# Performance work log

Hardware: AMD Instinct MI355X
Metric: run time of the kernel (lower is better)

The kernel has to match this reference:

```python
import jax, jax.numpy as jnp
import numpy as np
from jax import lax
from jax.scipy.special import gammaln

B, T_FEATS, T_TEXT = 16, 2000, 400
ADIM, ODIM = 256, 512
BIG_NEG = -1e30
BLANK_LOGP = -1.0  # log(blank_prob) with blank_prob = e**-1


def _conv1d(x, w, b, pad):
    # x: (B, C_in, L), w: (C_out, C_in, K)
    y = lax.conv_general_dilated(x, w, (1,), [(pad, pad)],
                                 dimension_numbers=('NCH', 'OIH', 'NCH'))
    return y + b[None, :, None]


def _betabinom_prior(T, N):
    # ESPnet AlignmentModule beta-binomial attention prior (w=1):
    # alpha_t = t (1..T), beta_t = T - t + 1, k = 1..N, n = N
    t = jnp.arange(1, T + 1, dtype=jnp.float32)
    a = t[:, None]                                   # (T,1)
    bb = (T - t + 1.0)[:, None]                      # (T,1)
    k = jnp.arange(1, N + 1, dtype=jnp.float32)[None, :]  # (1,N)
    n = float(N)
    betaln = lambda x, y: gammaln(x) + gammaln(y) - gammaln(x + y)
    logC = gammaln(n + 1.0) - gammaln(k + 1.0) - gammaln(n - k + 1.0)
    return logC + betaln(k + a, n - k + bb) - betaln(a, bb)  # (T,N)


def _alignment_encoder(txt, speech, tw1, tb1, tw2, tb2, fw1, fb1, fw2, fb2, fw3, fb3):
    t = txt.transpose(0, 2, 1)                       # (B, adim, T_text)
    t = jax.nn.relu(_conv1d(t, tw1, tb1, 1))
    t = _conv1d(t, tw2, tb2, 0)
    t = t.transpose(0, 2, 1)                         # (B, T_text, adim)

    f = speech.transpose(0, 2, 1)                    # (B, odim, T_feats)
    f = jax.nn.relu(_conv1d(f, fw1, fb1, 1))
    f = jax.nn.relu(_conv1d(f, fw2, fb2, 1))
    f = _conv1d(f, fw3, fb3, 0)
    f = f.transpose(0, 2, 1)                         # (B, T_feats, adim)

    # score = -||f_t - t_s||_2 via expansion (avoids (B,T,S,D) intermediate)
    d2 = (jnp.sum(f * f, -1)[:, :, None] + jnp.sum(t * t, -1)[:, None, :]
          - 2.0 * jnp.einsum('btd,bsd->bts', f, t))
    score = -jnp.sqrt(jnp.maximum(d2, 1e-12))        # (B, T_feats, T_text)
    logp = jax.nn.log_softmax(score, axis=-1)
    return logp + _betabinom_prior(T_FEATS, T_TEXT)[None]


def _forwardsum_loss(log_p_attn):
    # CTC forward algorithm; targets are 1..N (all distinct) + interleaved blanks
    Bv, T, N = log_p_attn.shape
    lp = jnp.concatenate(
        [jnp.full((Bv, T, 1), BLANK_LOGP, log_p_attn.dtype), log_p_attn], axis=-1)
    lp = jax.nn.log_softmax(lp, axis=-1)             # (B, T, N+1)
    S = 2 * N + 1
    ext = np.zeros(S, np.int32); ext[1::2] = np.arange(1, N + 1)
    skip_ok = np.zeros(S, bool); skip_ok[3::2] = True  # non-blank, distinct labels
    ext = jnp.asarray(ext); skip_ok = jnp.asarray(skip_ok)

    emit = lp[:, :, ext]                             # (B, T, S)
    alpha = jnp.full((Bv, S), BIG_NEG)
    alpha = alpha.at[:, 0].set(emit[:, 0, 0]).at[:, 1].set(emit[:, 0, 1])

    def step(alpha, e):
        a1 = jnp.concatenate([jnp.full((Bv, 1), BIG_NEG), alpha[:, :-1]], axis=1)
        a2 = jnp.concatenate([jnp.full((Bv, 2), BIG_NEG), alpha[:, :-2]], axis=1)
        a2 = jnp.where(skip_ok[None, :], a2, BIG_NEG)
        alpha = jnp.logaddexp(jnp.logaddexp(alpha, a1), a2) + e
        return alpha, None

    alpha, _ = lax.scan(step, alpha, jnp.moveaxis(emit[:, 1:], 1, 0))
    nll = -jnp.logaddexp(alpha[:, -1], alpha[:, -2])  # (B,)
    # F.ctc_loss reduction='mean' divides each sample's nll by target length
    return jnp.mean(nll / N)


def _mas_single(lp):
    # lp: (T_feats, T_text) -> monotonic alignment (T_feats,) int32
    log_prob = lp.T                                  # (N, T)
    N, T = T_TEXT, T_FEATS
    q0 = jnp.where(jnp.arange(N) == 0, log_prob[0, 0], BIG_NEG)

    def fwd(q, col):
        q = jnp.maximum(q, jnp.concatenate([jnp.full((1,), BIG_NEG), q[:-1]])) + col
        return q, q

    _, qs = lax.scan(fwd, q0, log_prob[:, 1:].T)     # (T-1, N)
    Q = lax.stop_gradient(jnp.concatenate([q0[None], qs], axis=0))  # (T, N)

    def bwd(a_next, q_col):
        i_a = jnp.maximum(a_next - 1, 0)
        a = jnp.where(a_next == 0, 0,
                      jnp.where(q_col[i_a] >= q_col[a_next], i_a, a_next))
        a = a.astype(jnp.int32)
        return a, a

    _, A_rev = lax.scan(bwd, jnp.array(N - 1, jnp.int32), Q[:-1], reverse=True)
    return jnp.concatenate([A_rev, jnp.array([N - 1], jnp.int32)])  # (T,)


def _viterbi_decode(log_p_attn):
    A = jax.vmap(_mas_single)(log_p_attn)            # (B, T_feats) int32
    ds = jax.vmap(lambda a: jnp.bincount(a, length=T_TEXT))(A)
    ds = ds.astype(log_p_attn.dtype)                 # (B, T_text) durations
    gathered = jnp.take_along_axis(log_p_attn, A[:, :, None], axis=2)[..., 0]
    bin_loss = -jnp.mean(jnp.mean(gathered, axis=1))
    return ds, bin_loss


def setup_inputs() -> dict:
    key = jax.random.key(0)
    ks = jax.random.split(key, 12)
    s = 0.05
    inp = {
        'speech': jax.random.normal(ks[0], (B, T_FEATS, ODIM), jnp.float32),
        'txt': jax.random.normal(ks[1], (B, T_TEXT, ADIM), jnp.float32),
        'speech_len': jnp.full((B,), T_FEATS, jnp.int32),
        'txt_len': jnp.full((B,), T_TEXT, jnp.int32),
        'tw1': jax.random.normal(ks[2], (ADIM, ADIM, 3)) * s,
        'tb1': jnp.zeros((ADIM,)),
        'tw2': jax.random.normal(ks[3], (ADIM, ADIM, 1)) * s,
        'tb2': jnp.zeros((ADIM,)),
        'fw1': jax.random.normal(ks[4], (ADIM, ODIM, 3)) * s,
        'fb1': jnp.zeros((ADIM,)),
        'fw2': jax.random.normal(ks[5], (ADIM, ADIM, 3)) * s,
        'fb2': jnp.zeros((ADIM,)),
        'fw3': jax.random.normal(ks[6], (ADIM, ADIM, 1)) * s,
        'fb3': jnp.zeros((ADIM,)),
    }
    return inp


def reference(speech, txt, speech_len, txt_len,
              tw1, tb1, tw2, tb2, fw1, fb1, fw2, fb2, fw3, fb3):
    # lengths are full (no padding), so masks are no-ops
    log_p_attn = _alignment_encoder(txt, speech, tw1, tb1, tw2, tb2,
                                    fw1, fb1, fw2, fb2, fw3, fb3)
    forwardsum_loss = _forwardsum_loss(log_p_attn)
    ds, bin_loss = _viterbi_decode(log_p_attn)
    return ds, bin_loss, forwardsum_loss, log_p_attn
```

## Files before the change

### kernel.cpp

```cpp
#include <hip/hip_runtime.h>
#include <math.h>

typedef unsigned int u32;
typedef unsigned long long u64;
typedef unsigned short u16;
typedef __attribute__((ext_vector_type(8))) _Float16 f16x8;
typedef __attribute__((ext_vector_type(4))) float f32x4;

#define BIGN (-1e30f)

static constexpr int NB = 16;
static constexpr int TF = 2000;
static constexpr int TT = 400;

__device__ __forceinline__ float wsum(float v){
#pragma unroll
  for(int o=32;o;o>>=1) v += __shfl_xor(v,o,64);
  return v;
}
__device__ __forceinline__ float EXP2(float x){ return __builtin_amdgcn_exp2f(x); }
__device__ __forceinline__ float LOG2(float x){ return __builtin_amdgcn_logf(x); }
__device__ __forceinline__ float lse2b(float x, float y){
  float m = fmaxf(x,y);
  return m + LOG2(1.0f + EXP2(-fabsf(x-y)));
}
__device__ __forceinline__ float lse3b(float x, float y, float z){
  float mx = fmaxf(fmaxf(x,y),z);
  float md = __builtin_amdgcn_fmed3f(x,y,z);
  float mn = fminf(fminf(x,y),z);
  return mx + LOG2(1.0f + EXP2(md-mx) + EXP2(mn-mx));
}
__device__ __forceinline__ u16 f2h(float v){
  _Float16 h = (_Float16)v;
  return *(u16*)&h;
}
__device__ __forceinline__ float shup1(float v){
  int r = __builtin_amdgcn_update_dpp(__float_as_int(BIGN), __float_as_int(v),
                                      0x138, 0xf, 0xf, false);
  return __int_as_float(r);
}

__global__ void k_lgt(double* lgt){
  int m = blockIdx.x*blockDim.x + threadIdx.x;
  if(m < 2432) lgt[m] = (m>=1)? lgamma((double)m) : 0.0;
}
__global__ void k_terms(const double* __restrict__ lgt, double* rowA, double* colA, double* sA){
  int i = blockIdx.x*blockDim.x + threadIdx.x;
  if(i < TF)   rowA[i] = -lgt[2401] - lgt[i+1] - lgt[2000-i] + lgt[2001];
  if(i < TT)   colA[i] =  lgt[401]  - lgt[i+2] - lgt[400-i];
  if(i < 2399) sA[i]   =  lgt[i+2]  + lgt[2399-i];
}

__device__ __forceinline__ void packf(const float* __restrict__ w, u16* __restrict__ dst,
    int CIN, int KW, int i){
  int k = i % KW;
  int c = (i / KW) % CIN;
  int o = i / (KW*CIN);
  dst[((size_t)k*256 + o)*CIN + c] = f2h(w[i]);
}
__device__ __forceinline__ void cvtp(const float* __restrict__ src, u16* __restrict__ dst,
    int P, int C, int i){
  int c = i % C;
  int p = (i / C) % (P+2);
  int b = i / (C*(P+2));
  float v = 0.f;
  if(p>=1 && p<=P) v = src[((size_t)b*P + (p-1))*C + c];
  dst[i] = f2h(v);
}
__device__ __forceinline__ void zpr(u16* __restrict__ buf, int P, int j){
  int c = j % 256;
  int s = (j / 256) & 1;
  int b = j / 512;
  buf[((size_t)b*(P+2) + (s? P+1 : 0))*256 + c] = 0;
}
__global__ __launch_bounds__(256) void prep1_k(
    const float* __restrict__ fw1, const float* __restrict__ fw2, const float* __restrict__ fw3,
    const float* __restrict__ tw1, const float* __restrict__ tw2, const float* __restrict__ txt,
    u16* fw1p, u16* fw2p, u16* fw3p, u16* tw1p, u16* tw2p,
    u16* inbfT, u16* tout1, u16* out1){
  constexpr int N = 393216+196608+65536+196608+65536+1646592+8192+8192;
  for(int i = blockIdx.x*256 + threadIdx.x; i < N; i += gridDim.x*256){
    int j = i;
    if(j < 393216){ packf(fw1, fw1p, 512, 3, j); continue; } j -= 393216;
    if(j < 196608){ packf(fw2, fw2p, 256, 3, j); continue; } j -= 196608;
    if(j < 65536) { packf(fw3, fw3p, 256, 1, j); continue; } j -= 65536;
    if(j < 196608){ packf(tw1, tw1p, 256, 3, j); continue; } j -= 196608;
    if(j < 65536) { packf(tw2, tw2p, 256, 1, j); continue; } j -= 65536;
    if(j < 1646592){ cvtp(txt, inbfT, TT, 256, j); continue; } j -= 1646592;
    if(j < 8192) { zpr(tout1, TT, j); continue; } j -= 8192;
    zpr(out1, TF, j);
  }
}

__global__ __launch_bounds__(256) void cvt_pad_k(const float* __restrict__ src, u16* __restrict__ dst,
    int P, int C){
  int n = NB*(P+2)*C;
  for(int i = blockIdx.x*256 + threadIdx.x; i < n; i += gridDim.x*256) cvtp(src, dst, P, C, i);
}
__global__ __launch_bounds__(256) void zpad_k(u16* __restrict__ buf, int P){
  int n = NB*2*256;
  for(int i = blockIdx.x*256 + threadIdx.x; i < n; i += gridDim.x*256) zpr(buf, P, i);
}

template<int CIN, int KW, bool RELU, bool OBF>
__global__ __launch_bounds__(256) void mfconv_k(const u16* __restrict__ inb,
    const u16* __restrict__ wp, const float* __restrict__ bias, void* __restrict__ outp, int P){
  __shared__ __align__(16) u16 Al[4*66*8];
  __shared__ __align__(16) u16 Bl[KW*4*256*8];
  const int b = blockIdx.y;
  const int m0 = blockIdx.x * 64;
  const int tid = threadIdx.x;
  const int lane = tid & 63, wv = tid >> 6;
  const int lo16 = lane & 15, hi = lane >> 4;
  constexpr int K1 = (KW==1)? 1 : 0;
  const u16* inB = inb + (size_t)b*(P+2)*CIN;
  f32x4 acc[4][4];
#pragma unroll
  for(int i=0;i<4;i++)
#pragma unroll
    for(int j=0;j<4;j++) acc[i][j] = (f32x4){0.f,0.f,0.f,0.f};

  for(int c0=0; c0<CIN; c0+=32){
    __syncthreads();
    for(int idx = tid; idx < 264; idx += 256){
      int r = idx >> 2, q = idx & 3;
      int rowp = m0 + r;
      f16x8 v = (f16x8){0,0,0,0,0,0,0,0};
      if(rowp <= P+1) v = *(const f16x8*)&inB[(size_t)rowp*CIN + c0 + q*8];
      *(f16x8*)&Al[(q*66 + r)*8] = v;
    }
#pragma unroll
    for(int k=0;k<KW;k++){
      const u16* wr = &wp[((size_t)(k*256) + tid)*CIN + c0];
      f16x8 w0 = *(const f16x8*)&wr[0];
      f16x8 w1 = *(const f16x8*)&wr[8];
      f16x8 w2 = *(const f16x8*)&wr[16];
      f16x8 w3 = *(const f16x8*)&wr[24];
      *(f16x8*)&Bl[((k*4+0)*256 + tid)*8] = w0;
      *(f16x8*)&Bl[((k*4+1)*256 + tid)*8] = w1;
      *(f16x8*)&Bl[((k*4+2)*256 + tid)*8] = w2;
      *(f16x8*)&Bl[((k*4+3)*256 + tid)*8] = w3;
    }
    __syncthreads();
#pragma unroll
    for(int k=0;k<KW;k++){
      f16x8 af[4];
#pragma unroll
      for(int rf=0;rf<4;rf++)
        af[rf] = *(const f16x8*)&Al[(hi*66 + rf*16 + lo16 + k + K1)*8];
#pragma unroll
      for(int cf=0;cf<4;cf++){
        int o = wv*64 + cf*16 + lo16;
        f16x8 bf = *(const f16x8*)&Bl[((k*4+hi)*256 + o)*8];
#pragma unroll
        for(int rf=0;rf<4;rf++)
          acc[rf][cf] = __builtin_amdgcn_mfma_f32_16x16x32_f16(af[rf], bf, acc[rf][cf], 0, 0, 0);
      }
    }
  }
#pragma unroll
  for(int cf=0;cf<4;cf++){
    int o = wv*64 + cf*16 + lo16;
    float bs = bias[o];
#pragma unroll
    for(int rf=0;rf<4;rf++){
#pragma unroll
      for(int j=0;j<4;j++){
        int p = m0 + rf*16 + hi*4 + j;
        if(p < P){
          float v = acc[rf][cf][j] + bs;
          if(RELU) v = fmaxf(v, 0.f);
          if(OBF) ((u16*)outp)[((size_t)b*(P+2) + p + 1)*256 + o] = f2h(v);
          else    ((float*)outp)[((size_t)b*P + p)*256 + o] = v;
        }
      }
    }
  }
}

__global__ __launch_bounds__(256) void norm2b_k(const float* __restrict__ x1, const float* __restrict__ x2,
    float* __restrict__ o1, float* __restrict__ o2){
  int r = blockIdx.x*4 + (threadIdx.x>>6);
  int lane = threadIdx.x & 63;
  const float* src; float* dst; int rr;
  if(r < NB*TF){ src = x1; dst = o1; rr = r; }
  else { rr = r - NB*TF; if(rr >= NB*TT) return; src = x2; dst = o2; }
  float4 v = ((const float4*)(src + (size_t)rr*256))[lane];
  float s = v.x*v.x + v.y*v.y + v.z*v.z + v.w*v.w;
  s = wsum(s);
  if(lane==0) dst[rr] = s;
}

__global__ __launch_bounds__(256) void score_gemm(const float* __restrict__ F, const float* __restrict__ Tn,
    const float* __restrict__ fn2, const float* __restrict__ tn2, float* __restrict__ outp){
  constexpr int KC = 32;
  __shared__ __align__(16) float As[KC][68];
  __shared__ __align__(16) float Bs[KC][68];
  const int b = blockIdx.z;
  const int t0 = blockIdx.y*64, s0 = blockIdx.x*64;
  const int tid = threadIdx.x, tx = tid&15, ty = tid>>4;
  const float* Fb = F  + (size_t)b*TF*256;
  const float* Tb = Tn + (size_t)b*TT*256;
  float acc[4][4] = {};
  const int lk = tid & 31, lt0 = (tid>>5)*8;
  for(int k0=0;k0<256;k0+=KC){
    __syncthreads();
#pragma unroll
    for(int i=0;i<8;i++){
      int t = t0 + lt0 + i;
      As[lk][lt0+i] = (t<TF)? Fb[(size_t)t*256 + k0 + lk] : 0.f;
      int s = s0 + lt0 + i;
      Bs[lk][lt0+i] = (s<TT)? Tb[(size_t)s*256 + k0 + lk] : 0.f;
    }
    __syncthreads();
#pragma unroll
    for(int k=0;k<KC;k++){
      float a0[4], b0[4];
      *(float4*)a0 = *(const float4*)&As[k][ty*4];
      *(float4*)b0 = *(const float4*)&Bs[k][tx*4];
#pragma unroll
      for(int i=0;i<4;i++)
#pragma unroll
        for(int j=0;j<4;j++) acc[i][j] = fmaf(a0[i], b0[j], acc[i][j]);
    }
  }
#pragma unroll
  for(int i=0;i<4;i++){
    int t = t0 + ty*4 + i;
    if(t<TF){
      float fn = fn2[b*TF + t];
#pragma unroll
      for(int j=0;j<4;j++){
        int s = s0 + tx*4 + j;
        if(s<TT){
          float d2 = fn + tn2[b*TT + s] - 2.f*acc[i][j];
          outp[((size_t)b*TF + t)*TT + s] = -sqrtf(fmaxf(d2, 1e-12f));
        }
      }
    }
  }
}

__global__ __launch_bounds__(128) void softmax_prior_k(float* __restrict__ logp,
    const double* __restrict__ rowA, const double* __restrict__ colA, const double* __restrict__ sA,
    float* __restrict__ Z2){
  const int row = blockIdx.x;
  const int t0 = row % TF;
  float* rp = logp + (size_t)row*TT;
  const int tid = threadIdx.x;
  __shared__ float sh2[2];
  float v[4]; int ix[4];
#pragma unroll
  for(int i=0;i<4;i++){ ix[i] = tid + i*128; v[i] = (ix[i]<TT)? rp[ix[i]] : BIGN; }
  float m = fmaxf(fmaxf(v[0],v[1]),fmaxf(v[2],v[3]));
#pragma unroll
  for(int o=32;o;o>>=1) m = fmaxf(m, __shfl_xor(m,o,64));
  if((tid&63)==0) sh2[tid>>6] = m;
  __syncthreads();
  m = fmaxf(sh2[0], sh2[1]);
  float s = 0.f;
#pragma unroll
  for(int i=0;i<4;i++) if(ix[i]<TT) s += __expf(v[i]-m);
  s = wsum(s);
  __syncthreads();
  if((tid&63)==0) sh2[tid>>6] = s;
  __syncthreads();
  s = sh2[0] + sh2[1];
  const float lse = m + __logf(s);
  const double rA = rowA[t0];
  float f[4]; float m2 = BIGN;
#pragma unroll
  for(int i=0;i<4;i++){
    if(ix[i]<TT){
      float pr = (float)(colA[ix[i]] + sA[t0+ix[i]] + rA);
      f[i] = (v[i]-lse) + pr;
      rp[ix[i]] = f[i];
      m2 = fmaxf(m2, f[i]);
    } else f[i] = BIGN;
  }
#pragma unroll
  for(int o=32;o;o>>=1) m2 = fmaxf(m2, __shfl_xor(m2,o,64));
  __syncthreads();
  if((tid&63)==0) sh2[tid>>6] = m2;
  __syncthreads();
  m2 = fmaxf(fmaxf(sh2[0],sh2[1]), -1.0f);
  float s2 = (tid==0)? __expf(-1.0f - m2) : 0.f;
#pragma unroll
  for(int i=0;i<4;i++) if(ix[i]<TT) s2 += __expf(f[i]-m2);
  s2 = wsum(s2);
  __syncthreads();
  if((tid&63)==0) sh2[tid>>6] = s2;
  __syncthreads();
  if(tid==0) Z2[row] = m2 + __logf(sh2[0]+sh2[1]);
}

#define LCTC8(E, KV) { \
  float bv = bnd[dir][((KV)-1)&1]; \
  float n1 = shup1(a[7]); \
  if(half && lane==0) n1 = bv; \
  float w0 = lse2b(a[0], n1); \
  float w1 = lse2b(a[2], a[1]); \
  float w2 = lse2b(a[4], a[3]); \
  float w3 = lse2b(a[6], a[5]); \
  a[7] = lse2b(a[7], w3) + (E)[3]; \
  a[5] = lse2b(a[5], w2) + (E)[2]; \
  a[3] = lse2b(a[3], w1) + (E)[1]; \
  a[1] = lse2b(a[1], w0) + (E)[0]; \
  a[6] = w3 + EBL; a[4] = w2 + EBL; a[2] = w1 + EBL; a[0] = w0 + EBL; \
  if(half==0 && lane==52) bnd[dir][(KV)&1] = a[7]; \
  __syncthreads(); }

#define CPREF4(E, K) { int kk=(K); if(kk>999) kk=999; int row = dir? (TF-1-kk) : kk; \
  const float* rpp = lp + (size_t)row*TT; \
  (E)[0]=rpp[jc[0]]*IL2; (E)[1]=rpp[jc[1]]*IL2; (E)[2]=rpp[jc[2]]*IL2; (E)[3]=rpp[jc[3]]*IL2; }

#define MAS_STEP(E, TIDX) { \
  float n1 = shup1(q[6]); \
  u32 byte = 0; \
  if(lane>0 && n1 >= q[0]) byte |= 1u; \
  if(q[0] >= q[1]) byte |= 2u; \
  if(q[1] >= q[2]) byte |= 4u; \
  if(q[2] >= q[3]) byte |= 8u; \
  if(q[3] >= q[4]) byte |= 16u; \
  if(q[4] >= q[5]) byte |= 32u; \
  if(q[5] >= q[6]) byte |= 64u; \
  cb[(size_t)((TIDX)-1)*64 + lane] = (unsigned char)byte; \
  q[6] = fmaxf(q[6], q[5]) + (E)[6]; \
  q[5] = fmaxf(q[5], q[4]) + (E)[5]; \
  q[4] = fmaxf(q[4], q[3]) + (E)[4]; \
  q[3] = fmaxf(q[3], q[2]) + (E)[3]; \
  q[2] = fmaxf(q[2], q[1]) + (E)[2]; \
  q[1] = fmaxf(q[1], q[0]) + (E)[1]; \
  q[0] = fmaxf(q[0], n1) + (E)[0]; }

#define MPREF(E, ROW) { int rr=(ROW); rr = (rr>TF-1)? (TF-1) : rr; const float* rpp = lp + (size_t)rr*TT; \
  (E)[0]=rpp[jc[0]]; (E)[1]=rpp[jc[1]]; (E)[2]=rpp[jc[2]]; (E)[3]=rpp[jc[3]]; \
  (E)[4]=rpp[jc[4]]; (E)[5]=rpp[jc[5]]; (E)[6]=rpp[jc[6]]; }

__global__ __launch_bounds__(256) __attribute__((amdgpu_waves_per_eu(1,1)))
void scan_k(const float* __restrict__ logp,
    const float* __restrict__ Z2, unsigned char* __restrict__ cmpb, float* __restrict__ nll){
  const int lane = threadIdx.x & 63;
  const int wave = threadIdx.x >> 6;
  constexpr float IL2 = 1.4426950408889634f;
  constexpr float L2  = 0.6931471805599453f;
  if(blockIdx.x < NB){
    const int b = blockIdx.x;
    const float* lp = logp + (size_t)b*TF*TT;
    __shared__ float af[801], ag[801];
    __shared__ float bnd[2][2];
    const int dir  = wave >> 1;
    const int half = wave & 1;
    const int base = half ? 424 : 0;
    double zs = 0.0;
    if(wave==0){
      for(int t=lane; t<TF; t+=64) zs += (double)Z2[b*TF + t];
#pragma unroll
      for(int o=32;o;o>>=1) zs += __shfl_xor(zs, o, 64);
    }
    int jc[4];
#pragma unroll
    for(int i=0;i<4;i++){
      int j = base/2 + 4*lane + i;
      if(dir) j = TT-1-j;
      jc[i] = (j < 0)? 0 : ((j > TT-1)? TT-1 : j);
    }
    float a[8];
#pragma unroll
    for(int i=0;i<8;i++) a[i] = BIGN;
    if(half==0 && lane==0){
      a[0] = -1.0f*IL2;
      a[1] = (dir? lp[(size_t)(TF-1)*TT + (TT-1)] : lp[0]) * IL2;
    }
    const float EBL = -1.0f*IL2;
    if(half==0 && lane==52) bnd[dir][0] = a[7];
    float e0[4],e1[4],e2[4],e3[4],e4[4],e5[4],e6[4],e7[4];
    CPREF4(e0,1); CPREF4(e1,2); CPREF4(e2,3); CPREF4(e3,4);
    CPREF4(e4,5); CPREF4(e5,6); CPREF4(e6,7); CPREF4(e7,8);
    __syncthreads();
    int k = 1;
    for(; k + 8 <= 993; k += 8){
      LCTC8(e0, k);   CPREF4(e0, k+8);
      LCTC8(e1, k+1); CPREF4(e1, k+9);
      LCTC8(e2, k+2); CPREF4(e2, k+10);
      LCTC8(e3, k+3); CPREF4(e3, k+11);
      LCTC8(e4, k+4); CPREF4(e4, k+12);
      LCTC8(e5, k+5); CPREF4(e5, k+13);
      LCTC8(e6, k+6); CPREF4(e6, k+14);
      LCTC8(e7, k+7); CPREF4(e7, k+15);
    }
    for(; k<=999; k++){
      float P[4];
      CPREF4(P, k);
      LCTC8(P, k);
    }
    float* dst = dir? ag : af;
#pragma unroll
    for(int i=0;i<8;i++){
      int s = base + 8*lane + i;
      if(half){ if(s<=800) dst[s] = a[i]; }
      else    { if(s<=423) dst[s] = a[i]; }
    }
    __syncthreads();
    if(wave==0){
      float acc = BIGN;
      for(int s = lane; s <= 800; s += 64){
        float x0 = af[s];
        float x1 = (s>=1)? af[s-1] : BIGN;
        float x2 = ((s&1) && s>=3)? af[s-2] : BIGN;
        float A1 = lse3b(x0,x1,x2);
        acc = lse2b(acc, A1 + ag[800-s]);
      }
#pragma unroll
      for(int o=32;o;o>>=1) acc = lse2b(acc, __shfl_xor(acc,o,64));
      if(lane==0) nll[b] = -((acc*L2) - (float)zs);
    }
  } else {
    if(wave) return;
    const int b = blockIdx.x - NB;
    const float* lp = logp + (size_t)b*TF*TT;
    unsigned char* cb = cmpb + (size_t)b*TF*64;
    int jc[7];
#pragma unroll
    for(int i=0;i<7;i++){ int j = 7*lane + i; jc[i] = (j < TT)? j : (TT-1); }
    float q[7];
#pragma unroll
    for(int i=0;i<7;i++) q[i] = BIGN;
    if(lane==0) q[0] = lp[0];
    float e0[7],e1[7],e2[7],e3[7];
    MPREF(e0,1); MPREF(e1,2); MPREF(e2,3); MPREF(e3,4);
    int t0 = 1;
    for(; t0 + 4 <= TF; t0 += 4){
      MAS_STEP(e0, t0);   MPREF(e0, t0+4);
      MAS_STEP(e1, t0+1); MPREF(e1, t0+5);
      MAS_STEP(e2, t0+2); MPREF(e2, t0+6);
      MAS_STEP(e3, t0+3); MPREF(e3, t0+7);
    }
    for(; t0<TF; t0++){
      float P[7];
      MPREF(P, t0);
      MAS_STEP(P, t0);
    }
    {
      float n1 = shup1(q[6]);
      u32 byte = 0;
      if(lane>0 && n1 >= q[0]) byte |= 1u;
      if(q[0] >= q[1]) byte |= 2u;
      if(q[1] >= q[2]) byte |= 4u;
      if(q[2] >= q[3]) byte |= 8u;
      if(q[3] >= q[4]) byte |= 16u;
      if(q[4] >= q[5]) byte |= 32u;
      if(q[5] >= q[6]) byte |= 64u;
      cb[(size_t)(TF-1)*64 + lane] = (unsigned char)byte;
    }
  }
}

__global__ __launch_bounds__(256) void masback_k(const unsigned char* __restrict__ cmpb,
    const float* __restrict__ logp, float* __restrict__ ds, float* __restrict__ gsum){
  const int b = blockIdx.x;
  const unsigned char* cb = cmpb + (size_t)b*TF*64;
  __shared__ unsigned char bits[500*64];
  __shared__ short Ash[TF];
  __shared__ int cnt[TT];
  __shared__ float ps[4];
  int a = TT-1;
  for(int ch=3; ch>=0; ch--){
    const int tlo = ch*500;
    __syncthreads();
    for(int i=threadIdx.x;i<8000;i+=256) ((u32*)bits)[i] = ((const u32*)(cb + (size_t)tlo*64))[i];
    __syncthreads();
    if(threadIdx.x==0){
      int thi = tlo + 499;
      if(ch==3){ Ash[TF-1] = (short)(TT-1); thi = TF-2; }
      for(int t=thi;t>=tlo;t--){
        if(a > 0){
          unsigned char w = bits[(t-tlo)*64 + a/7];
          a -= (int)((w >> (a%7)) & 1u);
        }
        Ash[t] = (short)a;
      }
    }
  }
  __syncthreads();
  for(int i=threadIdx.x;i<TT;i+=256) cnt[i]=0;
  __syncthreads();
  float part = 0.f;
  const float* lp = logp + (size_t)b*TF*TT;
  for(int t=threadIdx.x;t<TF;t+=256){
    int at = Ash[t];
    atomicAdd(&cnt[at], 1);
    part += lp[(size_t)t*TT + at];
  }
  __syncthreads();
  for(int i=threadIdx.x;i<TT;i+=256) ds[(size_t)b*TT + i] = (float)cnt[i];
  part = wsum(part);
  if((threadIdx.x&63)==0) ps[threadIdx.x>>6] = part;
  __syncthreads();
  if(threadIdx.x==0) gsum[b] = ps[0]+ps[1]+ps[2]+ps[3];
}

__global__ void final_k(const float* __restrict__ nll, const float* __restrict__ gsum, float* __restrict__ out){
  if(threadIdx.x==0 && blockIdx.x==0){
    float fs=0.f, bs=0.f;
    for(int b=0;b<NB;b++){ fs += nll[b] / (float)TT; bs += gsum[b] / (float)TF; }
    out[6400] = -(bs / (float)NB);
    out[6401] = fs / (float)NB;
  }
}

extern "C" void kernel_launch(void* const* d_in, const int* in_sizes, int n_in,
                              void* d_out, int out_size, void* d_ws, size_t ws_size,
                              hipStream_t stream){
  const float* speech = (const float*)d_in[0];
  const float* txt    = (const float*)d_in[1];
  const float* tw1 = (const float*)d_in[4];
  const float* tb1 = (const float*)d_in[5];
  const float* tw2 = (const float*)d_in[6];
  const float* tb2 = (const float*)d_in[7];
  const float* fw1 = (const float*)d_in[8];
  const float* fb1 = (const float*)d_in[9];
  const float* fw2 = (const float*)d_in[10];
  const float* fb2 = (const float*)d_in[11];
  const float* fw3 = (const float*)d_in[12];
  const float* fb3 = (const float*)d_in[13];
  float* out  = (float*)d_out;
  float* ds   = out;
  float* logp = out + 6402;
  char* ws = (char*)d_ws;
  double* lgt  = (double*)(ws + 0);
  double* rowA = (double*)(ws + 20480);
  double* colA = (double*)(ws + 36864);
  double* sA   = (double*)(ws + 40960);
  float*  nll  = (float*)(ws + 61440);
  float*  gsum = (float*)(ws + 61696);
  float*  Z2   = (float*)(ws + 65536);
  float*  fn2  = (float*)(ws + 196608);
  float*  tn2  = (float*)(ws + 327680);
  unsigned char* cmpb = (unsigned char*)(ws + 360448);
  float*  tenc = (float*)(ws + 2408448);
  float*  f1   = (float*)(ws + 8962048);
  if(ws_size < 41730048) return;

  char* lr = (char*)(((uintptr_t)logp + 255) & ~(uintptr_t)255);
  u16* inbfT = (u16*)lr;
  u16* tout1 = (u16*)(lr + 4000000);
  u16* inbfA = (u16*)lr;
  u16* out2  = (u16*)lr;
  u16* wbase = (u16*)(lr + 32900000);
  u16* fw1p = wbase;
  u16* fw2p = wbase + 393216;
  u16* fw3p = wbase + 589824;
  u16* tw1p = wbase + 655360;
  u16* tw2p = wbase + 851968;
  u16* out1  = (u16*)(lr + 34750000);

  k_lgt  <<<10,256,0,stream>>>(lgt);
  k_terms<<<10,256,0,stream>>>(lgt,rowA,colA,sA);

  prep1_k<<<2048,256,0,stream>>>(fw1,fw2,fw3,tw1,tw2, txt,
                                 fw1p,fw2p,fw3p,tw1p,tw2p, inbfT, tout1, out1);

  mfconv_k<256,3,true ,true ><<<dim3(7,NB),256,0,stream>>>(inbfT, tw1p, tb1, tout1, TT);
  mfconv_k<256,1,false,false><<<dim3(7,NB),256,0,stream>>>(tout1, tw2p, tb2, tenc, TT);

  cvt_pad_k<<<4096,256,0,stream>>>(speech, inbfA, TF, 512);
  mfconv_k<512,3,true ,true ><<<dim3(32,NB),256,0,stream>>>(inbfA, fw1p, fb1, out1, TF);
  zpad_k<<<32,256,0,stream>>>(out2, TF);
  mfconv_k<256,3,true ,true ><<<dim3(32,NB),256,0,stream>>>(out1, fw2p, fb2, out2, TF);
  mfconv_k<256,1,false,false><<<dim3(32,NB),256,0,stream>>>(out2, fw3p, fb3, f1, TF);

  norm2b_k<<<(NB*TF+NB*TT)/4,256,0,stream>>>(f1, tenc, fn2, tn2);

  score_gemm<<<dim3(7,32,NB),256,0,stream>>>(f1, tenc, fn2, tn2, logp);
  softmax_prior_k<<<NB*TF,128,0,stream>>>(logp, rowA, colA, sA, Z2);

  scan_k<<<2*NB,256,0,stream>>>(logp, Z2, cmpb, nll);
  masback_k<<<NB,256,0,stream>>>(cmpb, logp, ds, gsum);
  final_k<<<1,64,0,stream>>>(nll, gsum, out);
}
```

Measured before the change: 818.6 us.

## Overlap CTC wave halves with halo lanes to sync once per eight steps

The forward/backward CTC scan, which splits the state vector across two waves, used to exchange one boundary value through shared memory and run __syncthreads after every time step. Now the second wave's range starts 16 states earlier, so two overlapping halo lanes recompute the dependency cone. The full 16-state halo is exchanged and the block synchronised only once every eight steps. This cuts barrier cost in the serial recurrence at the price of some redundant lane work and a more complex, error-prone boundary handoff.

```diff
diff --git a/kernel.cpp b/kernel.cpp
--- a/kernel.cpp
+++ b/kernel.cpp
@@ -294,10 +294,8 @@
   if(tid==0) Z2[row] = m2 + __logf(sh2[0]+sh2[1]);
 }
 
-#define LCTC8(E, KV) { \
-  float bv = bnd[dir][((KV)-1)&1]; \
+#define LCTC8(E) { \
   float n1 = shup1(a[7]); \
-  if(half && lane==0) n1 = bv; \
   float w0 = lse2b(a[0], n1); \
   float w1 = lse2b(a[2], a[1]); \
   float w2 = lse2b(a[4], a[3]); \
@@ -306,9 +304,7 @@
   a[5] = lse2b(a[5], w2) + (E)[2]; \
   a[3] = lse2b(a[3], w1) + (E)[1]; \
   a[1] = lse2b(a[1], w0) + (E)[0]; \
-  a[6] = w3 + EBL; a[4] = w2 + EBL; a[2] = w1 + EBL; a[0] = w0 + EBL; \
-  if(half==0 && lane==52) bnd[dir][(KV)&1] = a[7]; \
-  __syncthreads(); }
+  a[6] = w3 + EBL; a[4] = w2 + EBL; a[2] = w1 + EBL; a[0] = w0 + EBL; }
 
 #define CPREF4(E, K) { int kk=(K); if(kk>999) kk=999; int row = dir? (TF-1-kk) : kk; \
   const float* rpp = lp + (size_t)row*TT; \
@@ -348,10 +344,10 @@
     const int b = blockIdx.x;
     const float* lp = logp + (size_t)b*TF*TT;
     __shared__ float af[801], ag[801];
-    __shared__ float bnd[2][2];
+    __shared__ float sb[2][2][16];
     const int dir  = wave >> 1;
     const int half = wave & 1;
-    const int base = half ? 424 : 0;
+    const int sbase = half ? 408 : 0;
     double zs = 0.0;
     if(wave==0){
       for(int t=lane; t<TF; t+=64) zs += (double)Z2[b*TF + t];
@@ -361,7 +357,7 @@
     int jc[4];
 #pragma unroll
     for(int i=0;i<4;i++){
-      int j = base/2 + 4*lane + i;
+      int j = sbase/2 + 4*lane + i;
       if(dir) j = TT-1-j;
       jc[i] = (j < 0)? 0 : ((j > TT-1)? TT-1 : j);
     }
@@ -373,32 +369,48 @@
       a[1] = (dir? lp[(size_t)(TF-1)*TT + (TT-1)] : lp[0]) * IL2;
     }
     const float EBL = -1.0f*IL2;
-    if(half==0 && lane==52) bnd[dir][0] = a[7];
+    if(half==0 && (lane==51 || lane==52)){
+#pragma unroll
+      for(int i=0;i<8;i++) sb[dir][0][(lane-51)*8+i] = a[i];
+    }
     float e0[4],e1[4],e2[4],e3[4],e4[4],e5[4],e6[4],e7[4];
     CPREF4(e0,1); CPREF4(e1,2); CPREF4(e2,3); CPREF4(e3,4);
     CPREF4(e4,5); CPREF4(e5,6); CPREF4(e6,7); CPREF4(e7,8);
     __syncthreads();
-    int k = 1;
-    for(; k + 8 <= 993; k += 8){
-      LCTC8(e0, k);   CPREF4(e0, k+8);
-      LCTC8(e1, k+1); CPREF4(e1, k+9);
-      LCTC8(e2, k+2); CPREF4(e2, k+10);
-      LCTC8(e3, k+3); CPREF4(e3, k+11);
-      LCTC8(e4, k+4); CPREF4(e4, k+12);
-      LCTC8(e5, k+5); CPREF4(e5, k+13);
-      LCTC8(e6, k+6); CPREF4(e6, k+14);
-      LCTC8(e7, k+7); CPREF4(e7, k+15);
+    int k = 1, kb = 0;
+    for(; k + 8 <= 1000; k += 8, kb++){
+      if(half && lane < 2){
+#pragma unroll
+        for(int i=0;i<8;i++) a[i] = sb[dir][kb&1][lane*8+i];
+      }
+      LCTC8(e0); CPREF4(e0, k+8);
+      LCTC8(e1); CPREF4(e1, k+9);
+      LCTC8(e2); CPREF4(e2, k+10);
+      LCTC8(e3); CPREF4(e3, k+11);
+      LCTC8(e4); CPREF4(e4, k+12);
+      LCTC8(e5); CPREF4(e5, k+13);
+      LCTC8(e6); CPREF4(e6, k+14);
+      LCTC8(e7); CPREF4(e7, k+15);
+      if(half==0 && (lane==51 || lane==52)){
+#pragma unroll
+        for(int i=0;i<8;i++) sb[dir][(kb+1)&1][(lane-51)*8+i] = a[i];
+      }
+      __syncthreads();
+    }
+    if(half && lane < 2){
+#pragma unroll
+      for(int i=0;i<8;i++) a[i] = sb[dir][kb&1][lane*8+i];
     }
     for(; k<=999; k++){
       float P[4];
       CPREF4(P, k);
-      LCTC8(P, k);
+      LCTC8(P);
     }
     float* dst = dir? ag : af;
 #pragma unroll
     for(int i=0;i<8;i++){
-      int s = base + 8*lane + i;
-      if(half){ if(s<=800) dst[s] = a[i]; }
+      int s = sbase + 8*lane + i;
+      if(half){ if(s>=424 && s<=800) dst[s] = a[i]; }
       else    { if(s<=423) dst[s] = a[i]; }
     }
     __syncthreads();
```

Result: no change. 819.2 us (+0.1%).

## Split CTC forward scan across four waves per direction with halo seams

Applied to the files above, without the earlier changes.

The forward-sum CTC scan now splits each direction's 801 states over four waves instead of two, with each lane holding 4 states instead of 8, so each lane does less serial work per time step. Instead of exchanging one boundary value with a block barrier every step, each wave recomputes a 16-state overlapping halo and copies the halo from its neighbour through shared memory, synchronising only once every 8 steps. The cost is redundant computation in the halo region, more waves per block (512 threads), and tighter register limits from the changed launch bounds.

```diff
diff --git a/kernel.cpp b/kernel.cpp
--- a/kernel.cpp
+++ b/kernel.cpp
@@ -294,25 +294,25 @@
   if(tid==0) Z2[row] = m2 + __logf(sh2[0]+sh2[1]);
 }
 
-#define LCTC8(E, KV) { \
-  float bv = bnd[dir][((KV)-1)&1]; \
-  float n1 = shup1(a[7]); \
-  if(half && lane==0) n1 = bv; \
+#define LCTC4(E) { \
+  float n1 = shup1(a[3]); \
   float w0 = lse2b(a[0], n1); \
   float w1 = lse2b(a[2], a[1]); \
-  float w2 = lse2b(a[4], a[3]); \
-  float w3 = lse2b(a[6], a[5]); \
-  a[7] = lse2b(a[7], w3) + (E)[3]; \
-  a[5] = lse2b(a[5], w2) + (E)[2]; \
   a[3] = lse2b(a[3], w1) + (E)[1]; \
   a[1] = lse2b(a[1], w0) + (E)[0]; \
-  a[6] = w3 + EBL; a[4] = w2 + EBL; a[2] = w1 + EBL; a[0] = w0 + EBL; \
-  if(half==0 && lane==52) bnd[dir][(KV)&1] = a[7]; \
-  __syncthreads(); }
-
-#define CPREF4(E, K) { int kk=(K); if(kk>999) kk=999; int row = dir? (TF-1-kk) : kk; \
+  a[2] = w1 + EBL; a[0] = w0 + EBL; }
+
+#define CPREF2(E, K) { int kk=(K); if(kk>999) kk=999; int row = dir? (TF-1-kk) : kk; \
   const float* rpp = lp + (size_t)row*TT; \
-  (E)[0]=rpp[jc[0]]*IL2; (E)[1]=rpp[jc[1]]*IL2; (E)[2]=rpp[jc[2]]*IL2; (E)[3]=rpp[jc[3]]*IL2; }
+  (E)[0]=rpp[jc0]*IL2; (E)[1]=rpp[jc1]*IL2; }
+
+#define SEAMW(BUF) if(q<3 && lane>=wl0 && lane<wl0+4){ \
+  float* sp = &sb[dir][q][BUF][(lane-wl0)*4]; \
+  sp[0]=a[0]; sp[1]=a[1]; sp[2]=a[2]; sp[3]=a[3]; }
+
+#define HALOR(BUF) if(q>0 && lane<4){ \
+  const float* sp = &sb[dir][q-1][BUF][lane*4]; \
+  a[0]=sp[0]; a[1]=sp[1]; a[2]=sp[2]; a[3]=sp[3]; }
 
 #define MAS_STEP(E, TIDX) { \
   float n1 = shup1(q[6]); \
@@ -337,7 +337,7 @@
   (E)[0]=rpp[jc[0]]; (E)[1]=rpp[jc[1]]; (E)[2]=rpp[jc[2]]; (E)[3]=rpp[jc[3]]; \
   (E)[4]=rpp[jc[4]]; (E)[5]=rpp[jc[5]]; (E)[6]=rpp[jc[6]]; }
 
-__global__ __launch_bounds__(256) __attribute__((amdgpu_waves_per_eu(1,1)))
+__global__ __launch_bounds__(512) __attribute__((amdgpu_waves_per_eu(2,2)))
 void scan_k(const float* __restrict__ logp,
     const float* __restrict__ Z2, unsigned char* __restrict__ cmpb, float* __restrict__ nll){
   const int lane = threadIdx.x & 63;
@@ -348,58 +348,61 @@
     const int b = blockIdx.x;
     const float* lp = logp + (size_t)b*TF*TT;
     __shared__ float af[801], ag[801];
-    __shared__ float bnd[2][2];
-    const int dir  = wave >> 1;
-    const int half = wave & 1;
-    const int base = half ? 424 : 0;
+    __shared__ float sb[2][3][2][16];
+    const int dir = wave >> 2;
+    const int q   = wave & 3;
+    const int sbase = (q==0)? 0 : 200*q - 16;
+    const int olo = 200*q;
+    const int ohi = (q<3)? 200*q+199 : 800;
+    const int wl0 = (q==0)? 46 : 50;
     double zs = 0.0;
     if(wave==0){
       for(int t=lane; t<TF; t+=64) zs += (double)Z2[b*TF + t];
 #pragma unroll
       for(int o=32;o;o>>=1) zs += __shfl_xor(zs, o, 64);
     }
-    int jc[4];
-#pragma unroll
-    for(int i=0;i<4;i++){
-      int j = base/2 + 4*lane + i;
-      if(dir) j = TT-1-j;
-      jc[i] = (j < 0)? 0 : ((j > TT-1)? TT-1 : j);
-    }
-    float a[8];
-#pragma unroll
-    for(int i=0;i<8;i++) a[i] = BIGN;
-    if(half==0 && lane==0){
+    int j0 = sbase/2 + 2*lane, j1 = j0 + 1;
+    if(dir){ j0 = TT-1-j0; j1 = TT-1-j1; }
+    const int jc0 = (j0<0)? 0 : ((j0>TT-1)? TT-1 : j0);
+    const int jc1 = (j1<0)? 0 : ((j1>TT-1)? TT-1 : j1);
+    float a[4];
+#pragma unroll
+    for(int i=0;i<4;i++) a[i] = BIGN;
+    if(q==0 && lane==0){
       a[0] = -1.0f*IL2;
       a[1] = (dir? lp[(size_t)(TF-1)*TT + (TT-1)] : lp[0]) * IL2;
     }
     const float EBL = -1.0f*IL2;
-    if(half==0 && lane==52) bnd[dir][0] = a[7];
-    float e0[4],e1[4],e2[4],e3[4],e4[4],e5[4],e6[4],e7[4];
-    CPREF4(e0,1); CPREF4(e1,2); CPREF4(e2,3); CPREF4(e3,4);
-    CPREF4(e4,5); CPREF4(e5,6); CPREF4(e6,7); CPREF4(e7,8);
-    __syncthreads();
-    int k = 1;
-    for(; k + 8 <= 993; k += 8){
-      LCTC8(e0, k);   CPREF4(e0, k+8);
-      LCTC8(e1, k+1); CPREF4(e1, k+9);
-      LCTC8(e2, k+2); CPREF4(e2, k+10);
-      LCTC8(e3, k+3); CPREF4(e3, k+11);
-      LCTC8(e4, k+4); CPREF4(e4, k+12);
-      LCTC8(e5, k+5); CPREF4(e5, k+13);
-      LCTC8(e6, k+6); CPREF4(e6, k+14);
-      LCTC8(e7, k+7); CPREF4(e7, k+15);
-    }
+    SEAMW(0);
+    float e0[2],e1[2],e2[2],e3[2],e4[2],e5[2],e6[2],e7[2];
+    CPREF2(e0,1); CPREF2(e1,2); CPREF2(e2,3); CPREF2(e3,4);
+    CPREF2(e4,5); CPREF2(e5,6); CPREF2(e6,7); CPREF2(e7,8);
+    __syncthreads();
+    int k = 1, kb = 0;
+    for(; k + 8 <= 1000; k += 8, kb++){
+      HALOR(kb&1);
+      LCTC4(e0); CPREF2(e0, k+8);
+      LCTC4(e1); CPREF2(e1, k+9);
+      LCTC4(e2); CPREF2(e2, k+10);
+      LCTC4(e3); CPREF2(e3, k+11);
+      LCTC4(e4); CPREF2(e4, k+12);
+      LCTC4(e5); CPREF2(e5, k+13);
+      LCTC4(e6); CPREF2(e6, k+14);
+      LCTC4(e7); CPREF2(e7, k+15);
+      SEAMW((kb+1)&1);
+      __syncthreads();
+    }
+    HALOR(kb&1);
     for(; k<=999; k++){
-      float P[4];
-      CPREF4(P, k);
-      LCTC8(P, k);
+      float P[2];
+      CPREF2(P, k);
+      LCTC4(P);
     }
     float* dst = dir? ag : af;
 #pragma unroll
-    for(int i=0;i<8;i++){
-      int s = base + 8*lane + i;
-      if(half){ if(s<=800) dst[s] = a[i]; }
-      else    { if(s<=423) dst[s] = a[i]; }
+    for(int i=0;i<4;i++){
+      int s = sbase + 4*lane + i;
+      if(s>=olo && s<=ohi) dst[s] = a[i];
     }
     __syncthreads();
     if(wave==0){
@@ -575,7 +578,7 @@
   score_gemm<<<dim3(7,32,NB),256,0,stream>>>(f1, tenc, fn2, tn2, logp);
   softmax_prior_k<<<NB*TF,128,0,stream>>>(logp, rowA, colA, sA, Z2);
 
-  scan_k<<<2*NB,256,0,stream>>>(logp, Z2, cmpb, nll);
+  scan_k<<<2*NB,512,0,stream>>>(logp, Z2, cmpb, nll);
   masback_k<<<NB,256,0,stream>>>(cmpb, logp, ds, gsum);
   final_k<<<1,64,0,stream>>>(nll, gsum, out);
 }
```

New measurement: 817.7 us. Within noise of the previous version (-0.1%).
